# Optimization experiments

Hardware: AMD Instinct MI355X
Metric: run time of the kernel (lower is better)

The kernel has to match this reference:

```python
import jax, jax.numpy as jnp
import numpy as np

N_INST, BATCH, IN_DIM, L_DIM = 256, 128, 1024, 512

def setup_inputs() -> dict:
    key = jax.random.key(0)
    k1, k2, k3, k4 = jax.random.split(key, 4)
    # glorot-uniform-ish scales
    sv = np.sqrt(6.0 / (IN_DIM + L_DIM)).astype(np.float32)
    sw = np.sqrt(6.0 / (L_DIM + 1)).astype(np.float32)
    x = jax.random.normal(k1, (N_INST, BATCH, IN_DIM), dtype=jnp.float32)
    v = jax.random.uniform(k2, (IN_DIM, L_DIM), minval=-sv, maxval=sv, dtype=jnp.float32)
    u = jax.random.uniform(k3, (IN_DIM, L_DIM), minval=-sv, maxval=sv, dtype=jnp.float32)
    w = jax.random.uniform(k4, (L_DIM, 1), minval=-sw, maxval=sw, dtype=jnp.float32)
    return {"x": x, "v": v, "u": u, "w": w}

def reference(x, v, u, w):
    # x: [n_instances, batch, in_dim]
    # Fused batched version of the per-instance loop:
    # score_i = (tanh(x_i @ v) * sigmoid(x_i @ u)) @ w, softmax over instances.
    h = jnp.tanh(jnp.einsum('nbd,dl->nbl', x, v))          # [n, b, l]
    g = jax.nn.sigmoid(jnp.einsum('nbd,dl->nbl', x, u))    # [n, b, l]
    scores = jnp.einsum('nbl,lo->nbo', h * g, w)            # [n, b, 1]
    alpha = jax.nn.softmax(scores, axis=0)                  # softmax over instance axis
    return alpha
```

## Files before the change

kernel.cpp:

```cpp
#include <hip/hip_runtime.h>
#include <stdint.h>

typedef unsigned int  u32;
typedef unsigned short u16;
typedef __bf16 v8bf __attribute__((ext_vector_type(8)));
typedef float  v4f  __attribute__((ext_vector_type(4)));

#define N_INST 256
#define BATCH  128
#define IN_DIM 1024
#define L_DIM  512
#define M_TOT  (N_INST*BATCH)
#define NSLICE 16

#define XB_BYTES   ((size_t)M_TOT * IN_DIM * 2)
#define WPK_BYTES  ((size_t)1024 * IN_DIM * 2)

__device__ inline u32 f2bf_pk(float a, float b){
  u32 ua = __builtin_bit_cast(u32, a);
  u32 ub = __builtin_bit_cast(u32, b);
  ua = (ua + 0x7FFFu + ((ua >> 16) & 1u)) >> 16;
  ub = (ub + 0x7FFFu + ((ub >> 16) & 1u)) & 0xFFFF0000u;
  return ua | ub;
}

#define PREP_XBLKS 16384
__global__ void prep(const float* __restrict__ x, const float* __restrict__ v,
                     const float* __restrict__ u, u16* __restrict__ xb,
                     u16* __restrict__ wpk){
  const int b = blockIdx.x;
  if (b < PREP_XBLKS){
    int t = b * 256 + threadIdx.x;
    int r = t >> 6, l = t & 63;
    int kk = r & 1, i = (r >> 1) & 3, h = (r >> 3) & 1, kt = (r >> 4) & 15, mb = r >> 8;
    int q = l >> 4, c = l & 15;
    int row = mb*128 + h*64 + i*16 + c;
    int k0  = kt*64 + kk*32 + q*8;
    const float* src = x + (size_t)row * IN_DIM + k0;
    float4 a0 = *reinterpret_cast<const float4*>(src);
    float4 a1 = *reinterpret_cast<const float4*>(src + 4);
    uint4 out;
    out.x = f2bf_pk(a0.x, a0.y); out.y = f2bf_pk(a0.z, a0.w);
    out.z = f2bf_pk(a1.x, a1.y); out.w = f2bf_pk(a1.z, a1.w);
    *reinterpret_cast<uint4*>(xb + (size_t)r*512 + l*8) = out;
  } else {
    int t = (b - PREP_XBLKS) * 256 + threadIdx.x;
    int r = t >> 6, l = t & 63;
    int kk = r & 1, j = (r >> 1) & 3, kt = (r >> 3) & 15, cs = r >> 7;
    int q = l >> 4, c = l & 15;
    int bcol = cs*4 + j;
    const float* src = (bcol & 1) ? u : v;
    int lcol = (bcol >> 1)*16 + c;
    int k0 = kt*64 + kk*32 + q*8;
    u32 o[4];
#pragma unroll
    for (int ii = 0; ii < 4; ++ii){
      float a  = src[(size_t)(k0 + 2*ii    ) * L_DIM + lcol];
      float bb = src[(size_t)(k0 + 2*ii + 1) * L_DIM + lcol];
      o[ii] = f2bf_pk(a, bb);
    }
    *reinterpret_cast<uint4*>(wpk + (size_t)r*512 + l*8) = make_uint4(o[0], o[1], o[2], o[3]);
  }
}


#define LOADA2(KT, KK, P) { const u16* ak_ = awave + (size_t)(KT)*8192 + (KK)*512;    \
  _Pragma("unroll") for (int gi_ = 0; gi_ < 4; ++gi_)                                 \
    af2[P][gi_] = *reinterpret_cast<const v8bf*>(ak_ + gi_*1024); }

#define LOADB2(KT, KK, P) { const u16* bk_ = bwave + (size_t)((KT)*8 + (KK))*512;     \
  _Pragma("unroll") for (int j_ = 0; j_ < 4; ++j_)                                    \
    bf2[P][j_] = *reinterpret_cast<const v8bf*>(bk_ + j_*1024); }

#define STEP_S(P, DO_R, NKT, NKK) {                                                   \
  __builtin_amdgcn_s_setprio(1);                                                      \
  _Pragma("unroll") for (int j_ = 0; j_ < 4; ++j_){                                   \
    _Pragma("unroll") for (int gi_ = 0; gi_ < 4; ++gi_)                               \
      acc[gi_][j_] = __builtin_amdgcn_mfma_f32_16x16x32_bf16(                         \
          af2[P][gi_], bf2[P][j_], acc[gi_][j_], 0, 0, 0);                            \
    if (DO_R) bf2[P][j_] = *reinterpret_cast<const v8bf*>(                            \
        bwave + (size_t)((NKT)*8 + j_*2 + (NKK))*512);                                \
  }                                                                                   \
  __builtin_amdgcn_s_setprio(0);                                                      \
  if (DO_R) LOADA2(NKT, NKK, P); }

__launch_bounds__(256, 3)
__global__ void gemm_score(const u16* __restrict__ xb, const u16* __restrict__ wpk,
                           const float* __restrict__ w, float* __restrict__ partial){
  const int tid  = threadIdx.x;
  const u32 bid  = blockIdx.x;
  const int xcd  = bid & 7;
  const int slot = bid >> 3;
  const int cs   = slot & 15;
  const int mr   = xcd*16 + (slot >> 4);
  const int mblk0= mr * 2;

  const int lane = tid & 63;
  const int wave = tid >> 6;
  const int q    = lane >> 4;
  const int c    = lane & 15;

  const u16* awave = xb + (size_t)(mblk0 + (wave>>1))*131072
                        + (size_t)((wave&1)*4)*1024 + lane*8;
  const u16* bwave = wpk + (size_t)cs*128*512 + lane*8;

  v8bf af2[2][4];
  v8bf bf2[2][4];
  v4f  acc[4][4];
#pragma unroll
  for (int gi = 0; gi < 4; ++gi)
#pragma unroll
    for (int j = 0; j < 4; ++j)
      acc[gi][j] = (v4f){0.f, 0.f, 0.f, 0.f};

  LOADB2(0, 0, 0); LOADA2(0, 0, 0);
  LOADB2(0, 1, 1); LOADA2(0, 1, 1);

#pragma unroll 1
  for (int kt = 0; kt < 15; ++kt){
    STEP_S(0, 1, kt+1, 0);
    STEP_S(1, 1, kt+1, 1);
  }
  STEP_S(0, 0, 0, 0);
  STEP_S(1, 0, 0, 0);

  const float wl0 = w[cs*32 + c];
  const float wl1 = w[cs*32 + 16 + c];
  float* pout = partial + (size_t)cs * M_TOT
              + (size_t)(mblk0 + (wave>>1))*128 + (wave&1)*64;

#pragma unroll
  for (int gi = 0; gi < 4; ++gi){
#pragma unroll
    for (int r = 0; r < 4; ++r){
      float t0 = 2.f / (1.f + __expf(-2.f * acc[gi][0][r])) - 1.f;
      float s0 = 1.f / (1.f + __expf(-acc[gi][1][r]));
      float t1 = 2.f / (1.f + __expf(-2.f * acc[gi][2][r])) - 1.f;
      float s1 = 1.f / (1.f + __expf(-acc[gi][3][r]));
      float v2 = t0*s0*wl0 + t1*s1*wl1;
      v2 += __shfl_xor(v2, 1, 64);
      v2 += __shfl_xor(v2, 2, 64);
      v2 += __shfl_xor(v2, 4, 64);
      v2 += __shfl_xor(v2, 8, 64);
      if (c == 0) pout[gi*16 + q*4 + r] = v2;
    }
  }
}

__global__ void softmax_inst(const float* __restrict__ partial, float* __restrict__ out){
  __shared__ float red[N_INST];
  const int b = blockIdx.x;
  const int n = threadIdx.x;
  float s = 0.f;
#pragma unroll
  for (int i = 0; i < NSLICE; ++i) s += partial[(size_t)i * M_TOT + n*BATCH + b];
  red[n] = s; __syncthreads();
  for (int st = N_INST/2; st > 0; st >>= 1){
    if (n < st) red[n] = fmaxf(red[n], red[n + st]);
    __syncthreads();
  }
  float mx = red[0]; __syncthreads();
  float e = __expf(s - mx);
  red[n] = e; __syncthreads();
  for (int st = N_INST/2; st > 0; st >>= 1){
    if (n < st) red[n] += red[n + st];
    __syncthreads();
  }
  out[n*BATCH + b] = e / red[0];
}

extern "C" void kernel_launch(void* const* d_in, const int* in_sizes, int n_in,
                              void* d_out, int out_size, void* d_ws, size_t ws_size,
                              hipStream_t stream) {
  const float* x = (const float*)d_in[0];
  const float* v = (const float*)d_in[1];
  const float* u = (const float*)d_in[2];
  const float* w = (const float*)d_in[3];
  u16*   xb      = (u16*)d_ws;
  u16*   wpk     = (u16*)((char*)d_ws + XB_BYTES);
  float* partial = (float*)((char*)d_ws + XB_BYTES + WPK_BYTES);
  float* out     = (float*)d_out;

  prep<<<dim3(PREP_XBLKS + 512), dim3(256), 0, stream>>>(x, v, u, xb, wpk);
  gemm_score<<<dim3(2048), dim3(256), 0, stream>>>(xb, wpk, w, partial);
  softmax_inst<<<dim3(BATCH), dim3(N_INST), 0, stream>>>(partial, out);
}
```

Baseline: 290.7 us.

## Stage A/B tiles through double-buffered LDS with async global-to-LDS loads

The GEMM now uses 512-thread blocks that cooperatively copy A and B k-tiles into a double-buffered LDS area with global_load_lds, then feed the MFMAs from LDS instead of loading each wave's fragments directly from global memory. Each block covers a 256-row by 64-column tile, so each staged tile is shared by several waves and global/L2 traffic per MFMA drops. The cost is a barrier plus a vmcnt(0) wait on every k step, 96 KB of LDS per block, and a different block-to-tile mapping, which together may limit occupancy and overlap.

```diff
diff --git a/kernel.cpp b/kernel.cpp
--- a/kernel.cpp
+++ b/kernel.cpp
@@ -22,6 +22,12 @@
   ua = (ua + 0x7FFFu + ((ua >> 16) & 1u)) >> 16;
   ub = (ub + 0x7FFFu + ((ub >> 16) & 1u)) & 0xFFFF0000u;
   return ua | ub;
+}
+
+__device__ inline void gl2lds16(const u16* g, u16* l){
+  __builtin_amdgcn_global_load_lds(
+      (const __attribute__((address_space(1))) u32*)(g),
+      (__attribute__((address_space(3))) u32*)(l), 16, 0, 0);
 }
 
 #define PREP_XBLKS 16384
@@ -64,48 +70,72 @@
 }
 
 
-#define LOADA2(KT, KK, P) { const u16* ak_ = awave + (size_t)(KT)*8192 + (KK)*512;    \
-  _Pragma("unroll") for (int gi_ = 0; gi_ < 4; ++gi_)                                 \
-    af2[P][gi_] = *reinterpret_cast<const v8bf*>(ak_ + gi_*1024); }
-
-#define LOADB2(KT, KK, P) { const u16* bk_ = bwave + (size_t)((KT)*8 + (KK))*512;     \
-  _Pragma("unroll") for (int j_ = 0; j_ < 4; ++j_)                                    \
-    bf2[P][j_] = *reinterpret_cast<const v8bf*>(bk_ + j_*1024); }
-
-#define STEP_S(P, DO_R, NKT, NKK) {                                                   \
+#define STAGE(KT, LB) { _Pragma("unroll") for (int it_ = 0; it_ < 6; ++it_)           \
+    gl2lds16(sp[it_] + (size_t)(KT)*sstr[it_], &Ls[(LB) + (wave*6+it_)*512]); }
+
+#define LOADA_F(P, LB, KK) { _Pragma("unroll") for (int gi_ = 0; gi_ < 4; ++gi_)      \
+    afb[P][gi_] = *reinterpret_cast<const v8bf*>(&Ls[(LB) + ao0 + (gi_*2+(KK))*512]); }
+
+#define LOADB_F(P, LB, KK) { _Pragma("unroll") for (int j_ = 0; j_ < 4; ++j_)         \
+    bfb[P][j_] = *reinterpret_cast<const v8bf*>(&Ls[(LB) + bo0 + (j_*2+(KK))*512]); }
+
+#define STEPX(P, DO_R, LB, NKK) {                                                     \
   __builtin_amdgcn_s_setprio(1);                                                      \
   _Pragma("unroll") for (int j_ = 0; j_ < 4; ++j_){                                   \
     _Pragma("unroll") for (int gi_ = 0; gi_ < 4; ++gi_)                               \
       acc[gi_][j_] = __builtin_amdgcn_mfma_f32_16x16x32_bf16(                         \
-          af2[P][gi_], bf2[P][j_], acc[gi_][j_], 0, 0, 0);                            \
-    if (DO_R) bf2[P][j_] = *reinterpret_cast<const v8bf*>(                            \
-        bwave + (size_t)((NKT)*8 + j_*2 + (NKK))*512);                                \
+          afb[P][gi_], bfb[P][j_], acc[gi_][j_], 0, 0, 0);                            \
+    if (DO_R) bfb[(P)^1][j_] = *reinterpret_cast<const v8bf*>(                        \
+        &Ls[(LB) + bo0 + (j_*2+(NKK))*512]);                                          \
   }                                                                                   \
   __builtin_amdgcn_s_setprio(0);                                                      \
-  if (DO_R) LOADA2(NKT, NKK, P); }
-
-__launch_bounds__(256, 3)
+  if (DO_R) LOADA_F((P)^1, LB, NKK); }
+
+#define WAIT_BAR {                                                                    \
+  __builtin_amdgcn_sched_barrier(0);                                                  \
+  asm volatile("s_waitcnt vmcnt(0)" ::: "memory");                                    \
+  __builtin_amdgcn_s_barrier();                                                       \
+  __builtin_amdgcn_sched_barrier(0); }
+
+__launch_bounds__(512, 2)
 __global__ void gemm_score(const u16* __restrict__ xb, const u16* __restrict__ wpk,
                            const float* __restrict__ w, float* __restrict__ partial){
+  __shared__ __align__(16) u16 Ls[2*48*512];
+
   const int tid  = threadIdx.x;
   const u32 bid  = blockIdx.x;
-  const int xcd  = bid & 7;
-  const int slot = bid >> 3;
-  const int cs   = slot & 15;
-  const int mr   = xcd*16 + (slot >> 4);
-  const int mblk0= mr * 2;
+  const int lo  = bid & 7;
+  const int csp = (bid >> 3) & 7;
+  const int hi  = bid >> 6;
+  const int m   = lo*16 + hi;
+  const int mblk0 = m*2;
 
   const int lane = tid & 63;
   const int wave = tid >> 6;
   const int q    = lane >> 4;
   const int c    = lane & 15;
-
-  const u16* awave = xb + (size_t)(mblk0 + (wave>>1))*131072
-                        + (size_t)((wave&1)*4)*1024 + lane*8;
-  const u16* bwave = wpk + (size_t)cs*128*512 + lane*8;
-
-  v8bf af2[2][4];
-  v8bf bf2[2][4];
+  const int wm   = wave >> 1;
+  const int wn   = wave & 1;
+
+  const u16* sp[6]; u32 sstr[6];
+#pragma unroll
+  for (int it = 0; it < 6; ++it){
+    int r = wave*6 + it;
+    if (r < 32){
+      sp[it]   = xb + ((size_t)(mblk0 + (r>>4))*256 + (r&15))*512 + lane*8;
+      sstr[it] = 16*512;
+    } else {
+      int rb = r - 32;
+      sp[it]   = wpk + ((size_t)((csp*2 + (rb>>3))*128 + (rb&7)))*512 + lane*8;
+      sstr[it] = 8*512;
+    }
+  }
+
+  const u32 ao0 = (u32)(((wm>>1)*16 + (wm&1)*8)*512) + lane*8;
+  const u32 bo0 = (u32)((32 + wn*8)*512) + lane*8;
+
+  v8bf afb[2][4];
+  v8bf bfb[2][4];
   v4f  acc[4][4];
 #pragma unroll
   for (int gi = 0; gi < 4; ++gi)
@@ -113,21 +143,23 @@
     for (int j = 0; j < 4; ++j)
       acc[gi][j] = (v4f){0.f, 0.f, 0.f, 0.f};
 
-  LOADB2(0, 0, 0); LOADA2(0, 0, 0);
-  LOADB2(0, 1, 1); LOADA2(0, 1, 1);
+  STAGE(0, 0);
+  u32 lb = 0;
 
 #pragma unroll 1
-  for (int kt = 0; kt < 15; ++kt){
-    STEP_S(0, 1, kt+1, 0);
-    STEP_S(1, 1, kt+1, 1);
-  }
-  STEP_S(0, 0, 0, 0);
-  STEP_S(1, 0, 0, 0);
-
+  for (int kt = 0; kt < 16; ++kt){
+    WAIT_BAR;
+    if (kt < 15) STAGE(kt+1, lb ^ 24576);
+    LOADA_F(0, lb, 0); LOADB_F(0, lb, 0);
+    STEPX(0, 1, lb, 1);
+    STEPX(1, 0, lb, 0);
+    lb ^= 24576;
+  }
+
+  const int cs = csp*2 + wn;
   const float wl0 = w[cs*32 + c];
   const float wl1 = w[cs*32 + 16 + c];
-  float* pout = partial + (size_t)cs * M_TOT
-              + (size_t)(mblk0 + (wave>>1))*128 + (wave&1)*64;
+  float* pout = partial + (size_t)cs * M_TOT + (size_t)m*256 + wm*64;
 
 #pragma unroll
   for (int gi = 0; gi < 4; ++gi){
@@ -182,6 +214,6 @@
   float* out     = (float*)d_out;
 
   prep<<<dim3(PREP_XBLKS + 512), dim3(256), 0, stream>>>(x, v, u, xb, wpk);
-  gemm_score<<<dim3(2048), dim3(256), 0, stream>>>(xb, wpk, w, partial);
+  gemm_score<<<dim3(1024), dim3(512), 0, stream>>>(xb, wpk, w, partial);
   softmax_inst<<<dim3(BATCH), dim3(N_INST), 0, stream>>>(partial, out);
 }
```

Measured after the change: 292.4 us. About the same (+0.6%).
